# Optimization experiments

Hardware: AMD Instinct MI355X
Metric: run time of the kernel (lower is better)

The kernel has to match this reference:

```python
import jax, jax.numpy as jnp
import numpy as np

E = 8       # num experts
TOPK = 2    # top-k routing
R = 16      # lora rank
D = 2048    # d_model
F = 5632    # ffn hidden
B, S = 4, 2048


def setup_inputs() -> dict:
    key = jax.random.key(0)
    ks = jax.random.split(key, 11)
    sc = 0.02
    return {
        "x": jax.random.normal(ks[0], (B, S, D), jnp.float32),
        "gate_w": jax.random.normal(ks[1], (E, D), jnp.float32) * sc,
        "W1": jax.random.normal(ks[2], (F, D), jnp.float32) * sc,
        "W3": jax.random.normal(ks[3], (F, D), jnp.float32) * sc,
        "W2": jax.random.normal(ks[4], (D, F), jnp.float32) * sc,
        "A1": jax.random.normal(ks[5], (E, R, D), jnp.float32) * sc,
        "B1": jax.random.normal(ks[6], (E, F, R), jnp.float32) * sc,
        "A3": jax.random.normal(ks[7], (E, R, D), jnp.float32) * sc,
        "B3": jax.random.normal(ks[8], (E, F, R), jnp.float32) * sc,
        "A2": jax.random.normal(ks[9], (E, R, F), jnp.float32) * sc,
        "B2": jax.random.normal(ks[10], (E, D, R), jnp.float32) * sc,
    }


def reference(x, gate_w, W1, W3, W2, A1, B1, A3, B3, A2, B2):
    b, s, d = x.shape
    h = x.reshape(-1, d)                              # [T, D] tokens
    # --- BasicMoe routing (fp32 softmax, top-k, renormalize) ---
    router_logits = h @ gate_w.T                      # [T, E]
    probs = jax.nn.softmax(router_logits.astype(jnp.float32), axis=-1)
    w, sel = jax.lax.top_k(probs, TOPK)               # [T, K]
    w = w / jnp.sum(w, axis=-1, keepdims=True)
    w = w.astype(h.dtype)
    # per-token per-expert combine coefficient [T, E] (0 if not routed)
    coef = jnp.sum(jax.nn.one_hot(sel, E, dtype=w.dtype) * w[..., None], axis=1)
    # --- shared base projections (expert-independent) ---
    base1 = h @ W1.T                                  # [T, F]
    base3 = h @ W3.T                                  # [T, F]
    out = jnp.zeros_like(h)
    # small fixed loop over experts; dense-masked equivalent of gather/scatter
    for e in range(E):
        u1 = base1 + (h @ A1[e].T) @ B1[e].T          # w1 + loraB1(loraA1(x))
        u3 = base3 + (h @ A3[e].T) @ B3[e].T
        g = jax.nn.silu(u1) * u3                      # SwiGLU gate
        y = g @ W2.T + (g @ A2[e].T) @ B2[e].T        # w2 + lora2
        out = out + coef[:, e:e + 1] * y
    return out.reshape(b, s, d), router_logits
```

## Files before the change

### kernel.cpp

```cpp
#include <hip/hip_runtime.h>
#include <hip/hip_bf16.h>
#include <stdint.h>

#define TT   8192
#define DD   2048
#define FF   5632
#define EE   8
#define RR   16
#define NALL 11520
#define NPAIR 16384

typedef float  f32x4  __attribute__((ext_vector_type(4)));
typedef __bf16 bf16x8 __attribute__((ext_vector_type(8)));
typedef __bf16 bf16x4 __attribute__((ext_vector_type(4)));

#define AS1CAST(p) ((__attribute__((address_space(1))) void*)(p))
#define AS3CAST(p) ((__attribute__((address_space(3))) void*)(p))

__global__ __launch_bounds__(256) void cvt_f32_bf16(const float* __restrict__ src,
                                                    __bf16* __restrict__ dst, int n4) {
    int stride = gridDim.x * 256;
    for (int i = blockIdx.x * 256 + threadIdx.x; i < n4; i += stride) {
        float4 v = ((const float4*)src)[i];
        bf16x4 o = {(__bf16)v.x, (__bf16)v.y, (__bf16)v.z, (__bf16)v.w};
        ((bf16x4*)dst)[i] = o;
    }
}

__global__ __launch_bounds__(256) void cvt_A13(const float* __restrict__ A1,
                                               const float* __restrict__ A3,
                                               __bf16* __restrict__ dst) {
    int i = blockIdx.x * 256 + threadIdx.x;
    int col4 = i & 511;
    int j = i >> 9;
    int e = j >> 5, l = j & 31;
    const float* src = (l < 16) ? (A1 + (size_t)(e * 16 + l) * DD)
                                : (A3 + (size_t)(e * 16 + (l - 16)) * DD);
    float4 v = ((const float4*)src)[col4];
    bf16x4 o = {(__bf16)v.x, (__bf16)v.y, (__bf16)v.z, (__bf16)v.w};
    ((bf16x4*)(dst + (size_t)j * DD))[col4] = o;
}

__global__ __launch_bounds__(256) void cvt_A2t(const float* __restrict__ A2,
                                               __bf16* __restrict__ A2t) {
    int i = blockIdx.x * 256 + threadIdx.x;
    int f = i % FF;
    int r = (i / FF) % RR;
    int e = i / (FF * RR);
    A2t[((size_t)e * FF + f) * RR + r] = (__bf16)A2[i];
}

__global__ __launch_bounds__(256) void router_k(const float* __restrict__ x,
                                                const float* __restrict__ gw,
                                                float* __restrict__ logits,
                                                int* __restrict__ pair_e,
                                                float* __restrict__ pair_w) {
    int t = blockIdx.x * 4 + (threadIdx.x >> 6);
    int lane = threadIdx.x & 63;
    const float* xr = x + (size_t)t * DD;
    float acc[EE];
#pragma unroll
    for (int e = 0; e < EE; e++) acc[e] = 0.f;
    for (int d = lane; d < DD; d += 64) {
        float xv = xr[d];
#pragma unroll
        for (int e = 0; e < EE; e++) acc[e] += xv * gw[e * DD + d];
    }
#pragma unroll
    for (int off = 32; off > 0; off >>= 1) {
#pragma unroll
        for (int e = 0; e < EE; e++) acc[e] += __shfl_down(acc[e], off, 64);
    }
    if (lane == 0) {
        float mx = acc[0];
#pragma unroll
        for (int e = 1; e < EE; e++) mx = fmaxf(mx, acc[e]);
        float p[EE];
#pragma unroll
        for (int e = 0; e < EE; e++) p[e] = __expf(acc[e] - mx);
        int e0 = 0;
#pragma unroll
        for (int e = 1; e < EE; e++) if (p[e] > p[e0]) e0 = e;
        int e1 = (e0 == 0) ? 1 : 0;
#pragma unroll
        for (int e = 0; e < EE; e++) if (e != e0 && p[e] > p[e1]) e1 = e;
        float s = p[e0] + p[e1];
        pair_e[2 * t] = e0;     pair_e[2 * t + 1] = e1;
        pair_w[2 * t] = p[e0] / s; pair_w[2 * t + 1] = p[e1] / s;
#pragma unroll
        for (int e = 0; e < EE; e++) logits[(size_t)t * EE + e] = acc[e];
    }
}

template <int OUT_BF16>
__global__ __launch_bounds__(512, 2) void gemm256(const __bf16* __restrict__ A,
                                                  const __bf16* __restrict__ B,
                                                  void* __restrict__ Cv,
                                                  int M, int N, int K) {
    __shared__ __align__(16) __bf16 lds[8][8192];
    char* const sbase = (char*)&lds[0][0];
    const int tid = threadIdx.x;
    const int w = tid >> 6, lane = tid & 63;
    const int lrow = lane & 15, lq = lane >> 4;
    const int wr = w >> 2, wc = w & 3;

    const int gx = gridDim.x;
    const int nwg = gx * gridDim.y;
    const int orig = blockIdx.x + blockIdx.y * gx;
    const int q8 = nwg >> 3, r8 = nwg & 7;
    const int xcd = orig & 7, sid = orig >> 3;
    const int nid = (xcd < r8 ? xcd * (q8 + 1) : r8 * (q8 + 1) + (xcd - r8) * q8) + sid;
    const int m0 = (nid % gx) * 256;
    const int n0 = (nid / gx) * 256;

    const size_t ldb = (size_t)K * 2;
    const int rq0 = w * 16 + (lane >> 3);
    const int cbs = ((lane & 7) * 16) ^ (((rq0 >> 2) & 1) << 5);
    const char* gA0 = (const char*)A + (size_t)(m0 + rq0) * ldb + cbs;
    const char* gA1 = gA0 + (size_t)128 * ldb;
    const char* gB0 = (const char*)B + (size_t)(n0 + rq0) * ldb + cbs;
    const char* gB1 = gB0 + (size_t)128 * ldb;
    const int wseg = w * 2048;

    const int sb = ((lrow >> 2) & 1) << 5;
    const int aoff = lrow * 128 + ((lq * 16) ^ sb);
    const int boff = ((wc & 1) * 64 + lrow) * 128 + ((lq * 16) ^ sb);
    const int abuf = wr;
    const int bbuf = 2 + (wc >> 1);

    f32x4 acc[8][4] = {};
    bf16x8 aR[4][2], aS[4][2], bR[2][2], bS[2][2];

#define GLDS(gp, lo) __builtin_amdgcn_global_load_lds(AS1CAST((void*)(gp)), AS3CAST(sbase + (lo)), 16, 0, 0)
#define STAGEM(gp, bufmh) do { const char* _g = (gp); \
        GLDS(_g, (bufmh) * 16384 + wseg); \
        GLDS(_g + 8 * ldb, (bufmh) * 16384 + wseg + 1024); } while (0)
#define LDAf(c, i, ks) (*(const bf16x8*)(sbase + ((c) * 4 + abuf) * 16384 + aoff + (i) * 2048 + (ks) * 64))
#define LDBf(c, j, ks) (*(const bf16x8*)(sbase + ((c) * 4 + bbuf) * 16384 + boff + (j) * 2048 + (ks) * 64))
#define MM(i, j, fa, fb) acc[i][j] = __builtin_amdgcn_mfma_f32_16x16x32_bf16(fa, fb, acc[i][j], 0, 0, 0)
#define PH_MID() do { __builtin_amdgcn_s_barrier(); \
        asm volatile("s_waitcnt lgkmcnt(0)" ::: "memory"); \
        __builtin_amdgcn_sched_barrier(0); \
        __builtin_amdgcn_s_setprio(1); } while (0)
#define PH_END() do { __builtin_amdgcn_s_setprio(0); \
        __builtin_amdgcn_s_barrier(); } while (0)

#define DO4(c, kBC, kAC) do { \
    _Pragma("unroll") for (int i = 0; i < 4; i++) { aR[i][0] = LDAf(c, i, 0); aR[i][1] = LDAf(c, i, 1); } \
    _Pragma("unroll") for (int j = 0; j < 2; j++) { bR[j][0] = LDBf(c, j, 0); bR[j][1] = LDBf(c, j, 1); } \
    STAGEM(gB0 + (size_t)(kBC) * 128, ((c) ^ 1) * 4 + 2); \
    PH_MID(); \
    _Pragma("unroll") for (int i = 0; i < 4; i++) \
    _Pragma("unroll") for (int j = 0; j < 2; j++) { MM(i, j, aR[i][0], bR[j][0]); MM(i, j, aR[i][1], bR[j][1]); } \
    PH_END(); \
    _Pragma("unroll") for (int i = 0; i < 4; i++) { aS[i][0] = LDAf(c, 4 + i, 0); aS[i][1] = LDAf(c, 4 + i, 1); } \
    STAGEM(gB1 + (size_t)(kBC) * 128, ((c) ^ 1) * 4 + 3); \
    PH_MID(); \
    _Pragma("unroll") for (int i = 0; i < 4; i++) \
    _Pragma("unroll") for (int j = 0; j < 2; j++) { MM(4 + i, j, aS[i][0], bR[j][0]); MM(4 + i, j, aS[i][1], bR[j][1]); } \
    PH_END(); \
    _Pragma("unroll") for (int j = 0; j < 2; j++) { bS[j][0] = LDBf(c, 2 + j, 0); bS[j][1] = LDBf(c, 2 + j, 1); } \
    STAGEM(gA0 + (size_t)(kAC) * 128, (c) * 4 + 0); \
    PH_MID(); \
    _Pragma("unroll") for (int i = 0; i < 4; i++) \
    _Pragma("unroll") for (int j = 0; j < 2; j++) { MM(i, 2 + j, aR[i][0], bS[j][0]); MM(i, 2 + j, aR[i][1], bS[j][1]); } \
    PH_END(); \
    STAGEM(gA1 + (size_t)(kAC) * 128, (c) * 4 + 1); \
    asm volatile("s_waitcnt vmcnt(4)" ::: "memory"); \
    PH_MID(); \
    _Pragma("unroll") for (int i = 0; i < 4; i++) \
    _Pragma("unroll") for (int j = 0; j < 2; j++) { MM(4 + i, 2 + j, aS[i][0], bS[j][0]); MM(4 + i, 2 + j, aS[i][1], bS[j][1]); } \
    PH_END(); \
} while (0)

    const int NT = K >> 6;
    const int NI = NT >> 1;

    STAGEM(gA0, 0); STAGEM(gA1, 1); STAGEM(gB0, 2); STAGEM(gB1, 3);
    STAGEM(gA0 + 128, 4); STAGEM(gA1 + 128, 5);
    asm volatile("s_waitcnt vmcnt(4)" ::: "memory");
    __builtin_amdgcn_s_barrier();

    for (int it = 0; it < NI; it++) {
        int k2 = 2 * it + 2; if (k2 > NT - 1) k2 = NT - 1;
        int k3 = 2 * it + 3; if (k3 > NT - 1) k3 = NT - 1;
        DO4(0, 2 * it + 1, k2);
        DO4(1, k2, k3);
    }

    asm volatile("s_waitcnt vmcnt(0)" ::: "memory");

#undef DO4
#undef PH_END
#undef PH_MID
#undef MM
#undef LDBf
#undef LDAf
#undef STAGEM
#undef GLDS

#pragma unroll
    for (int i = 0; i < 8; i++)
#pragma unroll
        for (int j = 0; j < 4; j++)
#pragma unroll
            for (int r = 0; r < 4; r++) {
                int row = m0 + wr * 128 + i * 16 + lq * 4 + r;
                int col = n0 + wc * 64 + j * 16 + lrow;
                float v = acc[i][j][r];
                if (OUT_BF16) ((__bf16*)Cv)[(size_t)row * N + col] = (__bf16)v;
                else          ((float*)Cv)[(size_t)row * N + col] = v;
            }
}

__global__ __launch_bounds__(256) void g_build_tok(const __bf16* __restrict__ base,
                                                   const __bf16* __restrict__ B1t,
                                                   const __bf16* __restrict__ B3t,
                                                   const __bf16* __restrict__ A2t,
                                                   const int* __restrict__ pair_e,
                                                   const float* __restrict__ pair_w,
                                                   __bf16* __restrict__ G,
                                                   float* __restrict__ GA,
                                                   int t0) {
    const int wave = threadIdx.x >> 6, lane = threadIdx.x & 63;
    const int lt = blockIdx.x * 4 + wave;
    const int t = t0 + lt;
    const int e0 = pair_e[2 * t], e1 = pair_e[2 * t + 1];
    const float w0 = pair_w[2 * t], w1 = pair_w[2 * t + 1];
    const __bf16* brow = base + (size_t)lt * NALL;

    float ha1a[16], ha3a[16], ha1b[16], ha3b[16];
    {
        const bf16x8* pa = (const bf16x8*)(brow + 2 * FF + e0 * 32);
        const bf16x8* pb = (const bf16x8*)(brow + 2 * FF + e1 * 32);
        bf16x8 a0 = pa[0], a1 = pa[1], a2v = pa[2], a3v = pa[3];
        bf16x8 b0 = pb[0], b1v = pb[1], b2v = pb[2], b3v = pb[3];
#pragma unroll
        for (int r = 0; r < 8; r++) {
            ha1a[r] = (float)a0[r];  ha1a[8 + r] = (float)a1[r];
            ha3a[r] = (float)a2v[r]; ha3a[8 + r] = (float)a3v[r];
            ha1b[r] = (float)b0[r];  ha1b[8 + r] = (float)b1v[r];
            ha3b[r] = (float)b2v[r]; ha3b[8 + r] = (float)b3v[r];
        }
    }
    const __bf16* B1a = B1t + (size_t)e0 * FF * RR;
    const __bf16* B3a = B3t + (size_t)e0 * FF * RR;
    const __bf16* A2a = A2t + (size_t)e0 * FF * RR;
    const __bf16* B1b = B1t + (size_t)e1 * FF * RR;
    const __bf16* B3b = B3t + (size_t)e1 * FF * RR;
    const __bf16* A2b = A2t + (size_t)e1 * FF * RR;
    __bf16* Grow = G + (size_t)lt * FF;

    float ga0[16], ga1[16];
#pragma unroll
    for (int r = 0; r < 16; r++) { ga0[r] = 0.f; ga1[r] = 0.f; }

    for (int f = lane; f < FF; f += 64) {
        const size_t fo = (size_t)f * RR;
        const bf16x8* p;
        p = (const bf16x8*)(B1a + fo); bf16x8 b1l = p[0], b1h = p[1];
        p = (const bf16x8*)(B3a + fo); bf16x8 b3l = p[0], b3h = p[1];
        p = (const bf16x8*)(B1b + fo); bf16x8 c1l = p[0], c1h = p[1];
        p = (const bf16x8*)(B3b + fo); bf16x8 c3l = p[0], c3h = p[1];
        float bb1 = (float)brow[f], bb3 = (float)brow[FF + f];
        float u1a = bb1, u3a = bb3, u1b = bb1, u3b = bb3;
#pragma unroll
        for (int r = 0; r < 8; r++) {
            u1a += ha1a[r] * (float)b1l[r] + ha1a[8 + r] * (float)b1h[r];
            u3a += ha3a[r] * (float)b3l[r] + ha3a[8 + r] * (float)b3h[r];
            u1b += ha1b[r] * (float)c1l[r] + ha1b[8 + r] * (float)c1h[r];
            u3b += ha3b[r] * (float)c3l[r] + ha3b[8 + r] * (float)c3h[r];
        }
        float g0 = (u1a / (1.f + __expf(-u1a))) * u3a;
        float g1 = (u1b / (1.f + __expf(-u1b))) * u3b;
        Grow[f] = (__bf16)(w0 * g0 + w1 * g1);
        p = (const bf16x8*)(A2a + fo); bf16x8 a2l = p[0], a2h = p[1];
        p = (const bf16x8*)(A2b + fo); bf16x8 a4l = p[0], a4h = p[1];
#pragma unroll
        for (int r = 0; r < 8; r++) {
            ga0[r]     += g0 * (float)a2l[r];
            ga0[8 + r] += g0 * (float)a2h[r];
            ga1[r]     += g1 * (float)a4l[r];
            ga1[8 + r] += g1 * (float)a4h[r];
        }
    }
#pragma unroll
    for (int off = 32; off > 0; off >>= 1) {
#pragma unroll
        for (int r = 0; r < 16; r++) {
            ga0[r] += __shfl_down(ga0[r], off, 64);
            ga1[r] += __shfl_down(ga1[r], off, 64);
        }
    }
    if (lane == 0) {
#pragma unroll
        for (int r = 0; r < 16; r++) {
            GA[(size_t)(2 * t) * RR + r]     = w0 * ga0[r];
            GA[(size_t)(2 * t + 1) * RR + r] = w1 * ga1[r];
        }
    }
}

__global__ __launch_bounds__(256) void combine_k(const float* __restrict__ Y,
                                                 const float* __restrict__ GA,
                                                 const float* __restrict__ B2,
                                                 const int* __restrict__ pair_e,
                                                 float* __restrict__ out,
                                                 int t0) {
    const int lt = blockIdx.x;
    const int t = t0 + lt;
    const int tid = threadIdx.x;
    __shared__ float g0[RR], g1[RR];
    if (tid < 16) g0[tid] = GA[(size_t)(2 * t) * RR + tid];
    else if (tid < 32) g1[tid - 16] = GA[(size_t)(2 * t + 1) * RR + (tid - 16)];
    __syncthreads();
    const int e0 = pair_e[2 * t], e1 = pair_e[2 * t + 1];
    const float* B2e0 = B2 + (size_t)e0 * DD * RR;
    const float* B2e1 = B2 + (size_t)e1 * DD * RR;
    for (int d = tid; d < DD; d += 256) {
        float l0 = 0.f, l1 = 0.f;
        const float4* b0 = (const float4*)(B2e0 + (size_t)d * RR);
        const float4* b1 = (const float4*)(B2e1 + (size_t)d * RR);
#pragma unroll
        for (int q = 0; q < 4; q++) {
            float4 v0 = b0[q], v1 = b1[q];
            l0 += g0[q * 4 + 0] * v0.x + g0[q * 4 + 1] * v0.y + g0[q * 4 + 2] * v0.z + g0[q * 4 + 3] * v0.w;
            l1 += g1[q * 4 + 0] * v1.x + g1[q * 4 + 1] * v1.y + g1[q * 4 + 2] * v1.z + g1[q * 4 + 3] * v1.w;
        }
        out[(size_t)t * DD + d] = Y[(size_t)lt * DD + d] + l0 + l1;
    }
}

extern "C" void kernel_launch(void* const* d_in, const int* in_sizes, int n_in,
                              void* d_out, int out_size, void* d_ws, size_t ws_size,
                              hipStream_t stream) {
    const float* x  = (const float*)d_in[0];
    const float* gw = (const float*)d_in[1];
    const float* W1 = (const float*)d_in[2];
    const float* W3 = (const float*)d_in[3];
    const float* W2 = (const float*)d_in[4];
    const float* A1 = (const float*)d_in[5];
    const float* B1 = (const float*)d_in[6];
    const float* A3 = (const float*)d_in[7];
    const float* B3 = (const float*)d_in[8];
    const float* A2 = (const float*)d_in[9];
    const float* B2 = (const float*)d_in[10];

    float* out    = (float*)d_out;
    float* logits = out + (size_t)TT * DD;

    char* ws = (char*)d_ws;
    size_t off = 0;
    auto carve = [&](size_t bytes) {
        char* p = ws + off;
        off += (bytes + 255) & ~(size_t)255;
        return p;
    };
    auto pad = [](size_t b) { return (b + 255) & ~(size_t)255; };

    __bf16* W2b   = (__bf16*)carve((size_t)DD * FF * 2);
    __bf16* B1b   = (__bf16*)carve((size_t)EE * FF * RR * 2);
    __bf16* B3b   = (__bf16*)carve((size_t)EE * FF * RR * 2);
    __bf16* A2t   = (__bf16*)carve((size_t)EE * FF * RR * 2);
    float*  GA    = (float*)carve((size_t)NPAIR * RR * 4);
    int*    pair_e = (int*)carve((size_t)NPAIR * 4);
    float*  pair_w = (float*)carve((size_t)NPAIR * 4);
    __bf16* W_all = (__bf16*)carve((size_t)NALL * DD * 2);
    __bf16* h_bf  = (__bf16*)carve((size_t)TT * DD * 2);
    float*  Y_full = (float*)W_all;
    size_t base0 = off;

    int C = 0, full = 0;
    {
        const int cand[6] = {8192, 4096, 2048, 1024, 512, 256};
        for (int ci = 0; ci < 6; ci++) {
            int c = cand[ci];
            size_t need = base0 + pad((size_t)TT * FF * 2) + pad((size_t)c * NALL * 2);
            if (need <= ws_size) { full = 1; C = c; break; }
        }
    }
    __bf16* Gbuf; __bf16* base_c; float* Y_c = nullptr;
    if (full) {
        Gbuf   = (__bf16*)carve((size_t)TT * FF * 2);
        base_c = (__bf16*)carve((size_t)C * NALL * 2);
    } else {
        C = 2048;
        while (C > 256) {
            size_t need = base0 + pad((size_t)C * NALL * 2) + pad((size_t)C * FF * 2);
            if (need <= ws_size) break;
            C >>= 1;
        }
        base_c = (__bf16*)carve((size_t)C * NALL * 2);
        Gbuf   = (__bf16*)carve((size_t)C * FF * 2);
        Y_c    = (float*)base_c;
    }

    cvt_f32_bf16<<<2048, 256, 0, stream>>>(x, h_bf, TT * DD / 4);
    cvt_f32_bf16<<<1024, 256, 0, stream>>>(W1, W_all, FF * DD / 4);
    cvt_f32_bf16<<<1024, 256, 0, stream>>>(W3, W_all + (size_t)FF * DD, FF * DD / 4);
    cvt_f32_bf16<<<1024, 256, 0, stream>>>(W2, W2b, DD * FF / 4);
    cvt_A13<<<512, 256, 0, stream>>>(A1, A3, W_all + (size_t)2 * FF * DD);
    cvt_f32_bf16<<<512, 256, 0, stream>>>(B1, B1b, EE * FF * RR / 4);
    cvt_f32_bf16<<<512, 256, 0, stream>>>(B3, B3b, EE * FF * RR / 4);
    cvt_A2t<<<EE * RR * FF / 256, 256, 0, stream>>>(A2, A2t);

    router_k<<<TT / 4, 256, 0, stream>>>(x, gw, logits, pair_e, pair_w);

    for (int t0 = 0; t0 < TT; t0 += C) {
        gemm256<1><<<dim3(C / 256, NALL / 256), 512, 0, stream>>>(
            h_bf + (size_t)t0 * DD, W_all, base_c, C, NALL, DD);
        __bf16* Gp = full ? (Gbuf + (size_t)t0 * FF) : Gbuf;
        g_build_tok<<<C / 4, 256, 0, stream>>>(base_c, B1b, B3b, A2t, pair_e, pair_w, Gp, GA, t0);
        if (!full) {
            gemm256<0><<<dim3(C / 256, DD / 256), 512, 0, stream>>>(
                Gbuf, W2b, Y_c, C, DD, FF);
            combine_k<<<C, 256, 0, stream>>>(Y_c, GA, B2, pair_e, out, t0);
        }
    }

    if (full) {
        gemm256<0><<<dim3(TT / 256, DD / 256), 512, 0, stream>>>(
            Gbuf, W2b, Y_full, TT, DD, FF);
        combine_k<<<TT, 256, 0, stream>>>(Y_full, GA, B2, pair_e, out, 0);
    }
}
```

Measured before the change: 1.500 ms.

## Fuse LoRA-B2 combine into W2 GEMM epilogue and chunk input conversion

Removes the separate combine kernel and the fp32 Y intermediate. The down-projection GEMM epilogue now adds the per-token B2 LoRA terms and writes straight to the output. The workspace is reorganised: x is converted to bf16 per chunk, and W2's bf16 copy reuses the W_all region once the first GEMM is done. This cuts a full write and read of Y and a launch, but the epilogue now does scattered B2 and GA loads per element, and C is capped at 4096, so the first GEMM may run in two chunks.

```diff
diff --git a/kernel.cpp b/kernel.cpp
--- a/kernel.cpp
+++ b/kernel.cpp
@@ -92,11 +92,15 @@
     }
 }
 
-template <int OUT_BF16>
+template <int MODE>
 __global__ __launch_bounds__(512, 2) void gemm256(const __bf16* __restrict__ A,
                                                   const __bf16* __restrict__ B,
                                                   void* __restrict__ Cv,
-                                                  int M, int N, int K) {
+                                                  int M, int N, int K,
+                                                  const float* __restrict__ GA,
+                                                  const float* __restrict__ B2,
+                                                  const int* __restrict__ pe,
+                                                  int tbase) {
     __shared__ __align__(16) __bf16 lds[8][8192];
     char* const sbase = (char*)&lds[0][0];
     const int tid = threadIdx.x;
@@ -199,18 +203,48 @@
 #undef STAGEM
 #undef GLDS
 
-#pragma unroll
-    for (int i = 0; i < 8; i++)
-#pragma unroll
-        for (int j = 0; j < 4; j++)
+    if (MODE == 1) {
+#pragma unroll
+        for (int i = 0; i < 8; i++)
+#pragma unroll
+            for (int j = 0; j < 4; j++)
+#pragma unroll
+                for (int r = 0; r < 4; r++) {
+                    int row = m0 + wr * 128 + i * 16 + lq * 4 + r;
+                    int col = n0 + wc * 64 + j * 16 + lrow;
+                    ((__bf16*)Cv)[(size_t)row * N + col] = (__bf16)acc[i][j][r];
+                }
+    } else {
+#pragma unroll
+        for (int i = 0; i < 8; i++) {
 #pragma unroll
             for (int r = 0; r < 4; r++) {
-                int row = m0 + wr * 128 + i * 16 + lq * 4 + r;
-                int col = n0 + wc * 64 + j * 16 + lrow;
-                float v = acc[i][j][r];
-                if (OUT_BF16) ((__bf16*)Cv)[(size_t)row * N + col] = (__bf16)v;
-                else          ((float*)Cv)[(size_t)row * N + col] = v;
+                const int row = m0 + wr * 128 + i * 16 + lq * 4 + r;
+                const int t = tbase + row;
+                const int e0 = pe[2 * t], e1 = pe[2 * t + 1];
+                const float4* g0p = (const float4*)(GA + (size_t)(2 * t) * RR);
+                const float4* g1p = (const float4*)(GA + (size_t)(2 * t + 1) * RR);
+                float4 ga0[4] = {g0p[0], g0p[1], g0p[2], g0p[3]};
+                float4 ga1[4] = {g1p[0], g1p[1], g1p[2], g1p[3]};
+                const float* B2e0 = B2 + (size_t)e0 * DD * RR;
+                const float* B2e1 = B2 + (size_t)e1 * DD * RR;
+#pragma unroll
+                for (int j = 0; j < 4; j++) {
+                    const int col = n0 + wc * 64 + j * 16 + lrow;
+                    float l = acc[i][j][r];
+                    const float4* b0 = (const float4*)(B2e0 + (size_t)col * RR);
+                    const float4* b1 = (const float4*)(B2e1 + (size_t)col * RR);
+#pragma unroll
+                    for (int q = 0; q < 4; q++) {
+                        float4 v0 = b0[q], v1 = b1[q];
+                        l += ga0[q].x * v0.x + ga0[q].y * v0.y + ga0[q].z * v0.z + ga0[q].w * v0.w;
+                        l += ga1[q].x * v1.x + ga1[q].y * v1.y + ga1[q].z * v1.z + ga1[q].w * v1.w;
+                    }
+                    ((float*)Cv)[(size_t)t * N + col] = l;
+                }
             }
+        }
+    }
 }
 
 __global__ __launch_bounds__(256) void g_build_tok(const __bf16* __restrict__ base,
@@ -301,36 +335,6 @@
     }
 }
 
-__global__ __launch_bounds__(256) void combine_k(const float* __restrict__ Y,
-                                                 const float* __restrict__ GA,
-                                                 const float* __restrict__ B2,
-                                                 const int* __restrict__ pair_e,
-                                                 float* __restrict__ out,
-                                                 int t0) {
-    const int lt = blockIdx.x;
-    const int t = t0 + lt;
-    const int tid = threadIdx.x;
-    __shared__ float g0[RR], g1[RR];
-    if (tid < 16) g0[tid] = GA[(size_t)(2 * t) * RR + tid];
-    else if (tid < 32) g1[tid - 16] = GA[(size_t)(2 * t + 1) * RR + (tid - 16)];
-    __syncthreads();
-    const int e0 = pair_e[2 * t], e1 = pair_e[2 * t + 1];
-    const float* B2e0 = B2 + (size_t)e0 * DD * RR;
-    const float* B2e1 = B2 + (size_t)e1 * DD * RR;
-    for (int d = tid; d < DD; d += 256) {
-        float l0 = 0.f, l1 = 0.f;
-        const float4* b0 = (const float4*)(B2e0 + (size_t)d * RR);
-        const float4* b1 = (const float4*)(B2e1 + (size_t)d * RR);
-#pragma unroll
-        for (int q = 0; q < 4; q++) {
-            float4 v0 = b0[q], v1 = b1[q];
-            l0 += g0[q * 4 + 0] * v0.x + g0[q * 4 + 1] * v0.y + g0[q * 4 + 2] * v0.z + g0[q * 4 + 3] * v0.w;
-            l1 += g1[q * 4 + 0] * v1.x + g1[q * 4 + 1] * v1.y + g1[q * 4 + 2] * v1.z + g1[q * 4 + 3] * v1.w;
-        }
-        out[(size_t)t * DD + d] = Y[(size_t)lt * DD + d] + l0 + l1;
-    }
-}
-
 extern "C" void kernel_launch(void* const* d_in, const int* in_sizes, int n_in,
                               void* d_out, int out_size, void* d_ws, size_t ws_size,
                               hipStream_t stream) {
@@ -358,69 +362,71 @@
     };
     auto pad = [](size_t b) { return (b + 255) & ~(size_t)255; };
 
-    __bf16* W2b   = (__bf16*)carve((size_t)DD * FF * 2);
     __bf16* B1b   = (__bf16*)carve((size_t)EE * FF * RR * 2);
     __bf16* B3b   = (__bf16*)carve((size_t)EE * FF * RR * 2);
     __bf16* A2t   = (__bf16*)carve((size_t)EE * FF * RR * 2);
     float*  GA    = (float*)carve((size_t)NPAIR * RR * 4);
     int*    pair_e = (int*)carve((size_t)NPAIR * 4);
     float*  pair_w = (float*)carve((size_t)NPAIR * 4);
-    __bf16* W_all = (__bf16*)carve((size_t)NALL * DD * 2);
-    __bf16* h_bf  = (__bf16*)carve((size_t)TT * DD * 2);
-    float*  Y_full = (float*)W_all;
+    char*   WREG  = carve((size_t)NALL * DD * 2);
+    __bf16* W_all = (__bf16*)WREG;
     size_t base0 = off;
 
     int C = 0, full = 0;
     {
-        const int cand[6] = {8192, 4096, 2048, 1024, 512, 256};
-        for (int ci = 0; ci < 6; ci++) {
+        const int cand[5] = {4096, 2048, 1024, 512, 256};
+        for (int ci = 0; ci < 5; ci++) {
             int c = cand[ci];
-            size_t need = base0 + pad((size_t)TT * FF * 2) + pad((size_t)c * NALL * 2);
+            size_t need = base0 + pad((size_t)TT * FF * 2)
+                        + pad((size_t)c * DD * 2) + pad((size_t)c * NALL * 2);
             if (need <= ws_size) { full = 1; C = c; break; }
         }
     }
-    __bf16* Gbuf; __bf16* base_c; float* Y_c = nullptr;
+    __bf16* Gbuf = nullptr; __bf16* base_c; __bf16* h_c; __bf16* W2b; __bf16* G_c = nullptr;
     if (full) {
         Gbuf   = (__bf16*)carve((size_t)TT * FF * 2);
+        h_c    = (__bf16*)carve((size_t)C * DD * 2);
         base_c = (__bf16*)carve((size_t)C * NALL * 2);
+        W2b    = (__bf16*)WREG;
     } else {
+        W2b = (__bf16*)carve((size_t)DD * FF * 2);
         C = 2048;
         while (C > 256) {
-            size_t need = base0 + pad((size_t)C * NALL * 2) + pad((size_t)C * FF * 2);
+            size_t need = off + pad((size_t)C * DD * 2)
+                        + pad((size_t)C * NALL * 2) + pad((size_t)C * FF * 2);
             if (need <= ws_size) break;
             C >>= 1;
         }
+        h_c    = (__bf16*)carve((size_t)C * DD * 2);
         base_c = (__bf16*)carve((size_t)C * NALL * 2);
-        Gbuf   = (__bf16*)carve((size_t)C * FF * 2);
-        Y_c    = (float*)base_c;
-    }
-
-    cvt_f32_bf16<<<2048, 256, 0, stream>>>(x, h_bf, TT * DD / 4);
+        G_c    = (__bf16*)carve((size_t)C * FF * 2);
+    }
+
     cvt_f32_bf16<<<1024, 256, 0, stream>>>(W1, W_all, FF * DD / 4);
     cvt_f32_bf16<<<1024, 256, 0, stream>>>(W3, W_all + (size_t)FF * DD, FF * DD / 4);
-    cvt_f32_bf16<<<1024, 256, 0, stream>>>(W2, W2b, DD * FF / 4);
     cvt_A13<<<512, 256, 0, stream>>>(A1, A3, W_all + (size_t)2 * FF * DD);
     cvt_f32_bf16<<<512, 256, 0, stream>>>(B1, B1b, EE * FF * RR / 4);
     cvt_f32_bf16<<<512, 256, 0, stream>>>(B3, B3b, EE * FF * RR / 4);
     cvt_A2t<<<EE * RR * FF / 256, 256, 0, stream>>>(A2, A2t);
+    if (!full) cvt_f32_bf16<<<1024, 256, 0, stream>>>(W2, W2b, DD * FF / 4);
 
     router_k<<<TT / 4, 256, 0, stream>>>(x, gw, logits, pair_e, pair_w);
 
     for (int t0 = 0; t0 < TT; t0 += C) {
+        cvt_f32_bf16<<<1024, 256, 0, stream>>>(x + (size_t)t0 * DD, h_c, C * DD / 4);
         gemm256<1><<<dim3(C / 256, NALL / 256), 512, 0, stream>>>(
-            h_bf + (size_t)t0 * DD, W_all, base_c, C, NALL, DD);
-        __bf16* Gp = full ? (Gbuf + (size_t)t0 * FF) : Gbuf;
+            h_c, W_all, base_c, C, NALL, DD, nullptr, nullptr, nullptr, 0);
+        __bf16* Gp = full ? (Gbuf + (size_t)t0 * FF) : G_c;
         g_build_tok<<<C / 4, 256, 0, stream>>>(base_c, B1b, B3b, A2t, pair_e, pair_w, Gp, GA, t0);
         if (!full) {
-            gemm256<0><<<dim3(C / 256, DD / 256), 512, 0, stream>>>(
-                Gbuf, W2b, Y_c, C, DD, FF);
-            combine_k<<<C, 256, 0, stream>>>(Y_c, GA, B2, pair_e, out, t0);
+            gemm256<2><<<dim3(C / 256, DD / 256), 512, 0, stream>>>(
+                G_c, W2b, out, C, DD, FF, GA, B2, pair_e, t0);
         }
     }
 
     if (full) {
-        gemm256<0><<<dim3(TT / 256, DD / 256), 512, 0, stream>>>(
-            Gbuf, W2b, Y_full, TT, DD, FF);
-        combine_k<<<TT, 256, 0, stream>>>(Y_full, GA, B2, pair_e, out, 0);
-    }
-}
+        cvt_f32_bf16<<<1024, 256, 0, stream>>>(W2, W2b, DD * FF / 4);
+        gemm256<2><<<dim3(TT / 256, DD / 256), 512, 0, stream>>>(
+            Gbuf, W2b, out, TT, DD, FF, GA, B2, pair_e, 0);
+    }
+}
```

New measurement: 1.353 ms. 9.7% less time.
